# Kernel tuning notes

Hardware: AMD Instinct MI355X
Metric: run time of the kernel (lower is better)

The kernel has to match this reference:

```python
import jax, jax.numpy as jnp
import numpy as np

B, TK, NK, H = 64, 512, 256, 512

def _masked_renorm_softmax(scores, mask):
    # softmax over last dim, multiply by mask, renormalize (as in the torch code)
    p = jax.nn.softmax(scores, axis=-1) * mask
    return p / jnp.sum(p, axis=-1, keepdims=True)

def setup_inputs() -> dict:
    key = jax.random.key(0)
    ks = jax.random.split(key, 14)
    s = 0.02
    return {
        "s_t_hat": jax.random.normal(ks[0], (B, 2 * H), jnp.float32),
        "encoder_outputs_token": jax.random.normal(ks[1], (B, TK, H), jnp.float32),
        "encoder_outputs_node": jax.random.normal(ks[2], (B, NK, H), jnp.float32),
        "node_to_token": jax.random.randint(ks[3], (B, TK), 0, NK),
        "enc_padding_mask_token": jnp.ones((B, TK), jnp.float32),
        "enc_padding_mask_node": jnp.ones((B, NK), jnp.float32),
        "graph": jax.random.uniform(ks[4], (B, NK, NK), jnp.float32),
        "flow": jax.random.uniform(ks[5], (B, NK), jnp.float32),
        # parameters (Linear weights stored as [in, out]; x @ W == torch Linear)
        "W_c": jax.random.normal(ks[6], (H,), jnp.float32) * s,          # Linear(1, H)
        "W_tok": jax.random.normal(ks[7], (H, H), jnp.float32) * s,      # encode_proj_token
        "W_node": jax.random.normal(ks[8], (H, H), jnp.float32) * s,     # encode_proj_node
        "W_dec": jax.random.normal(ks[9], (2 * H, H), jnp.float32) * s,  # decode_proj
        "b_dec": jnp.zeros((H,), jnp.float32),
        "v_tok": jax.random.normal(ks[10], (H,), jnp.float32) * s,       # v_token
        "v_node": jax.random.normal(ks[11], (H,), jnp.float32) * s,      # v_node
    }

def reference(s_t_hat, encoder_outputs_token, encoder_outputs_node, node_to_token,
              enc_padding_mask_token, enc_padding_mask_node, graph, flow,
              W_c, W_tok, W_node, W_dec, b_dec, v_tok, v_node):
    # projections
    enc_tok_feat = jnp.einsum('bth,hk->btk', encoder_outputs_token, W_tok)   # [B,TK,H]
    enc_node_feat = jnp.einsum('bnh,hk->bnk', encoder_outputs_node, W_node)  # [B,NK,H]
    dec_fea = s_t_hat @ W_dec + b_dec                                        # [B,H]
    flow_feat = flow[..., None] * W_c                                        # [B,NK,H]

    # node attention
    e_node = jnp.tanh(enc_node_feat + dec_fea[:, None, :] + flow_feat)
    scores_node = jnp.einsum('bnh,h->bn', e_node, v_node)                    # [B,NK]
    attn_dist_node = _masked_renorm_softmax(scores_node, enc_padding_mask_node)

    # gather node attention onto tokens via node_to_token indices
    gathered = jnp.take_along_axis(attn_dist_node, node_to_token, axis=1)    # [B,TK]
    attn_dist_node_to_token = _masked_renorm_softmax(gathered, enc_padding_mask_token)

    # token attention
    e_tok = jnp.tanh(enc_tok_feat + dec_fea[:, None, :])
    scores_tok = jnp.einsum('bth,h->bt', e_tok, v_tok)                       # [B,TK]
    attn_dist_token = _masked_renorm_softmax(scores_tok, enc_padding_mask_token)

    # mix and context
    final_attn = 0.5 * attn_dist_token + 0.5 * attn_dist_node_to_token      # [B,TK]
    c_t = jnp.einsum('bt,bth->bh', final_attn, encoder_outputs_token)        # [B,H]

    # multi-hop graph diffusion of node attention
    zero_hop = attn_dist_node                                                # [B,NK]
    one_hop = jnp.einsum('bn,bnm->bm', zero_hop, graph)
    two_hop = jnp.einsum('bn,bnm->bm', one_hop, graph)
    flow_out = (zero_hop + one_hop + two_hop) * 0.33333

    return (c_t, final_attn, attn_dist_node, flow_out)
```

## Files before the change

kernel.cpp:

```cpp
#include <hip/hip_runtime.h>
#include <math.h>

constexpr int kB = 64;
constexpr int kTK = 512;
constexpr int kNK = 256;
constexpr int kH = 512;
constexpr int kTokBlocks = kB * kTK / 64;
constexpr int kNodeBlocks = kB * kNK / 64;

typedef float f32x4 __attribute__((ext_vector_type(4)));
typedef __bf16 bf16x8 __attribute__((ext_vector_type(8)));

__device__ __forceinline__ unsigned short f32_to_bf16(float f) {
  return (unsigned short)((__float_as_uint(f) + 0x8000u) >> 16);
}

__device__ __forceinline__ float tanh_fast(float x) {
  float e = __builtin_amdgcn_exp2f(x * 2.8853900817779268f);
  return 1.0f - 2.0f * __builtin_amdgcn_rcpf(e + 1.0f);
}

__device__ __forceinline__ void lds_barrier() {
  __builtin_amdgcn_s_waitcnt(0xC07F);
  __builtin_amdgcn_s_barrier();
}

__global__ __launch_bounds__(256) void prep_kernel(
    const float* __restrict__ Wtok, const float* __restrict__ Wnode,
    unsigned short* __restrict__ WtokT, unsigned short* __restrict__ WnodeT,
    const float* __restrict__ s_t_hat, const float* __restrict__ W_dec,
    float* __restrict__ dec_part) {
  __shared__ float sm[32 * 33];
  const int tid = threadIdx.x;
  if (blockIdx.x < 512) {
    const int idx = blockIdx.x;
    const int z = idx >> 8, rem = idx & 255;
    const int bx = rem & 15, by = rem >> 4;
    const float* W = z ? Wnode : Wtok;
    unsigned short* T = z ? WnodeT : WtokT;
    const int tx = tid & 31, ty = tid >> 5;
#pragma unroll
    for (int i = 0; i < 4; ++i)
      sm[(ty + 8 * i) * 33 + tx] =
          W[(size_t)(by * 32 + ty + 8 * i) * kH + bx * 32 + tx];
    __syncthreads();
#pragma unroll
    for (int i = 0; i < 4; ++i)
      T[(size_t)(bx * 32 + ty + 8 * i) * kH + by * 32 + tx] =
          f32_to_bf16(sm[tx * 33 + ty + 8 * i]);
  } else {
    const int r = blockIdx.x - 512;
    const int b = r >> 3, s = r & 7;
    if (tid < 128) sm[tid] = s_t_hat[(size_t)b * 1024 + s * 128 + tid];
    __syncthreads();
    float a0 = 0.f, a1 = 0.f;
    const float* w = W_dec + (size_t)(s * 128) * kH;
#pragma unroll 8
    for (int k = 0; k < 128; ++k) {
      a0 = fmaf(sm[k], w[(size_t)k * kH + tid], a0);
      a1 = fmaf(sm[k], w[(size_t)k * kH + tid + 256], a1);
    }
    dec_part[(size_t)(b * 8 + s) * kH + tid] = a0;
    dec_part[(size_t)(b * 8 + s) * kH + tid + 256] = a1;
  }
}

__global__ __launch_bounds__(1024, 4) void scores_fused_kernel(
    const float* __restrict__ enc_tok, const float* __restrict__ enc_node,
    const unsigned short* __restrict__ WtokT,
    const unsigned short* __restrict__ WnodeT,
    const float* __restrict__ dec_part, const float* __restrict__ b_dec,
    const float* __restrict__ flow, const float* __restrict__ W_c,
    const float* __restrict__ v_tok, const float* __restrict__ v_node,
    float* __restrict__ scores_tok, float* __restrict__ scores_node) {
  const int tid = threadIdx.x;
  const int wave = tid >> 6, lane = tid & 63;
  const int quad = lane >> 4, l15 = lane & 15;
  const bool is_node = blockIdx.x >= kTokBlocks;
  const int bidx = is_node ? (int)blockIdx.x - kTokBlocks : (int)blockIdx.x;
  const float* A = is_node ? enc_node : enc_tok;
  const unsigned short* WT = is_node ? WnodeT : WtokT;
  const float* v = is_node ? v_node : v_tok;
  float* scores = is_node ? scores_node : scores_tok;
  const int ROWS = is_node ? kNK : kTK;
  const int b = is_node ? (bidx >> 2) : (bidx >> 3);
  const int row0 = (is_node ? (bidx & 3) : (bidx & 7)) * 64;

  __shared__ __align__(16) unsigned short As[2][8192];
  __shared__ float red[16][64];

  const f32x4 fzero = {0.f, 0.f, 0.f, 0.f};
  f32x4 acc[4][2];
#pragma unroll
  for (int i = 0; i < 4; ++i)
#pragma unroll
    for (int j = 0; j < 2; ++j) acc[i][j] = fzero;

  const int r = tid >> 4;
  const int kcol = tid & 15;
  const float* aptr = A + (size_t)(b * ROWS + row0 + r) * kH + kcol * 4;
  const int k0 = kcol * 4;
  const int k1 = 64 + kcol * 4;
  const int s0 = ((k0 >> 5) * 4 + (r >> 4)) * 64 + ((k0 >> 3) & 3) * 16 + (r & 15);
  const int s1 = ((k1 >> 5) * 4 + (r >> 4)) * 64 + ((k1 >> 3) & 3) * 16 + (r & 15);
  const int sw0 = s0 ^ (((s0 >> 4) & 3) << 1) ^ ((s0 >> 8) & 1);
  const int sw1 = s1 ^ (((s1 >> 4) & 3) << 1) ^ ((s1 >> 8) & 1);
  const int addr0 = sw0 * 8 + (k0 & 7);
  const int addr1 = sw1 * 8 + (k1 & 7);

  float4 axA0, axA1, axB0, axB1;
  auto aloadA = [&](int kc) {
    axA0 = *(const float4*)(aptr + kc * 128);
    axA1 = *(const float4*)(aptr + kc * 128 + 64);
  };
  auto aloadB = [&](int kc) {
    axB0 = *(const float4*)(aptr + kc * 128);
    axB1 = *(const float4*)(aptr + kc * 128 + 64);
  };
  auto commit = [&](int buf, float4 x0, float4 x1) {
    ushort4 h0, h1;
    h0.x = f32_to_bf16(x0.x); h0.y = f32_to_bf16(x0.y);
    h0.z = f32_to_bf16(x0.z); h0.w = f32_to_bf16(x0.w);
    h1.x = f32_to_bf16(x1.x); h1.y = f32_to_bf16(x1.y);
    h1.z = f32_to_bf16(x1.z); h1.w = f32_to_bf16(x1.w);
    *(ushort4*)&As[buf][addr0] = h0;
    *(ushort4*)&As[buf][addr1] = h1;
  };

  const int n0 = wave * 32;
  const unsigned short* bbase = WT + (size_t)(n0 + l15) * kH + quad * 8;
  bf16x8 bbuf[4][2];
  auto loadB = [&](int sb, int g) {
    bbuf[sb][0] = *(const bf16x8*)(bbase + g * 32);
    bbuf[sb][1] = *(const bf16x8*)(bbase + (size_t)16 * kH + g * 32);
  };

  aloadA(0);
  aloadB(1);
  loadB(0, 0);
  loadB(1, 1);
  loadB(2, 2);
  commit(0, axA0, axA1);
  aloadA(2);
  lds_barrier();

#pragma unroll
  for (int g = 0; g < 16; ++g) {
    const int kc = g >> 2, kh = g & 3;
    if (g == 0) { commit(1, axB0, axB1); aloadB(3); }
    else if (g == 4) { commit(0, axA0, axA1); }
    else if (g == 8) { commit(1, axB0, axB1); }
    if (g < 13) loadB((g + 3) & 3, g + 3);
    bf16x8 afr[4];
#pragma unroll
    for (int mi = 0; mi < 4; ++mi) {
      const int slot = ((kh * 4 + mi) * 64 + lane) ^ (((lane >> 4) & 3) << 1) ^ (kh & 1);
      afr[mi] = *(const bf16x8*)&As[kc & 1][slot * 8];
    }
#pragma unroll
    for (int mi = 0; mi < 4; ++mi)
#pragma unroll
      for (int ni = 0; ni < 2; ++ni)
        acc[mi][ni] = __builtin_amdgcn_mfma_f32_16x16x32_bf16(
            afr[mi], bbuf[g & 3][ni], acc[mi][ni], 0, 0, 0);
    if (kh == 3 && kc < 3) lds_barrier();
  }

  float dec2[2], vv2[2], wc2[2];
#pragma unroll
  for (int ni = 0; ni < 2; ++ni) {
    const int col = n0 + 16 * ni + l15;
    float d = b_dec[col];
#pragma unroll
    for (int p = 0; p < 8; ++p) d += dec_part[(size_t)(b * 8 + p) * kH + col];
    dec2[ni] = d;
    vv2[ni] = v[col];
    wc2[ni] = is_node ? W_c[col] : 0.f;
  }
#pragma unroll
  for (int mi = 0; mi < 4; ++mi) {
#pragma unroll
    for (int reg = 0; reg < 4; ++reg) {
      const int row = 16 * mi + quad * 4 + reg;
      const float fl = is_node ? flow[b * kNK + row0 + row] : 0.f;
      float p = 0.f;
#pragma unroll
      for (int ni = 0; ni < 2; ++ni)
        p += tanh_fast(fmaf(fl, wc2[ni], acc[mi][ni][reg] + dec2[ni])) * vv2[ni];
#pragma unroll
      for (int off = 1; off < 16; off <<= 1) p += __shfl_xor(p, off, 64);
      if (l15 == 0) red[wave][row] = p;
    }
  }
  __syncthreads();
  if (tid < 64) {
    float s = 0.f;
#pragma unroll
    for (int w = 0; w < 16; ++w) s += red[w][tid];
    scores[b * ROWS + row0 + tid] = s;
  }
}

__device__ __forceinline__ float block_sum_512(float v, float* rbuf) {
#pragma unroll
  for (int off = 32; off >= 1; off >>= 1) v += __shfl_xor(v, off, 64);
  if ((threadIdx.x & 63) == 0) rbuf[threadIdx.x >> 6] = v;
  __syncthreads();
  float s = rbuf[0];
#pragma unroll
  for (int w = 1; w < 8; ++w) s += rbuf[w];
  __syncthreads();
  return s;
}

__global__ __launch_bounds__(512) void softmax_mix_kernel(
    const float* __restrict__ scores_node, const float* __restrict__ scores_tok,
    const int* __restrict__ node_to_token,
    const float* __restrict__ mask_tok, const float* __restrict__ mask_node,
    float* __restrict__ out_final, float* __restrict__ out_attn_node,
    float* __restrict__ out_flow) {
  const int b = blockIdx.x, tid = threadIdx.x;
  __shared__ float an_sh[kNK];
  __shared__ float rbuf[8];

  if (tid < kNK) out_flow[b * kNK + tid] = 0.f;

  float en = 0.f;
  if (tid < kNK)
    en = expf(scores_node[b * kNK + tid]) * mask_node[b * kNK + tid];
  float sn = block_sum_512(en, rbuf);
  float an = en / sn;
  if (tid < kNK) {
    an_sh[tid] = an;
    out_attn_node[b * kNK + tid] = an;
  }
  __syncthreads();

  const float mt = mask_tok[b * kTK + tid];
  const int idx = node_to_token[b * kTK + tid];
  float eg = expf(an_sh[idx]) * mt;
  float sg = block_sum_512(eg, rbuf);
  float an2t = eg / sg;

  float et = expf(scores_tok[b * kTK + tid]) * mt;
  float st = block_sum_512(et, rbuf);
  float at = et / st;

  out_final[b * kTK + tid] = 0.5f * (at + an2t);
}

__global__ __launch_bounds__(512) void ct_flow1_kernel(
    const float* __restrict__ final_attn, const float* __restrict__ enc_tok,
    const float* __restrict__ attn_node, const float* __restrict__ graph,
    float* __restrict__ ctp, float* __restrict__ fp1) {
  const int tid = threadIdx.x;
  if (blockIdx.x < 512) {
    const int b = blockIdx.x >> 3, s = blockIdx.x & 7;
    __shared__ float fa[64];
    __shared__ float part[4][512];
    if (tid < 64) fa[tid] = final_attn[b * kTK + s * 64 + tid];
    __syncthreads();
    const int h4 = (tid & 127) * 4, tsub = tid >> 7;
    float4 acc = {0.f, 0.f, 0.f, 0.f};
    const float* base =
        enc_tok + ((size_t)(b * kTK + s * 64 + tsub * 16)) * kH + h4;
#pragma unroll
    for (int t = 0; t < 16; ++t) {
      float4 e = *(const float4*)(base + (size_t)t * kH);
      const float w = fa[tsub * 16 + t];
      acc.x = fmaf(w, e.x, acc.x); acc.y = fmaf(w, e.y, acc.y);
      acc.z = fmaf(w, e.z, acc.z); acc.w = fmaf(w, e.w, acc.w);
    }
    *(float4*)&part[tsub][h4] = acc;
    __syncthreads();
    if (tid < 128) {
      float4 s0 = {0.f, 0.f, 0.f, 0.f};
#pragma unroll
      for (int p = 0; p < 4; ++p) {
        float4 pp = *(const float4*)&part[p][tid * 4];
        s0.x += pp.x; s0.y += pp.y; s0.z += pp.z; s0.w += pp.w;
      }
      *(float4*)&ctp[((size_t)(b * 8 + s)) * kH + tid * 4] = s0;
    }
  } else {
    const int rr = blockIdx.x - 512;
    const int b = rr >> 2, sl = rr & 3;
    __shared__ float z[64];
    __shared__ float part[8][256];
    if (tid < 64) z[tid] = attn_node[b * kNK + sl * 64 + tid];
    __syncthreads();
    const int m4 = (tid & 63) * 4, nsub = tid >> 6;
    float4 acc = {0.f, 0.f, 0.f, 0.f};
    const float* g =
        graph + ((size_t)(b * kNK + sl * 64 + nsub * 8)) * kNK + m4;
#pragma unroll
    for (int n = 0; n < 8; ++n) {
      float4 gg = *(const float4*)(g + (size_t)n * kNK);
      const float w = z[nsub * 8 + n];
      acc.x = fmaf(w, gg.x, acc.x); acc.y = fmaf(w, gg.y, acc.y);
      acc.z = fmaf(w, gg.z, acc.z); acc.w = fmaf(w, gg.w, acc.w);
    }
    *(float4*)&part[nsub][m4] = acc;
    __syncthreads();
    if (tid < 64) {
      float4 s0 = {0.f, 0.f, 0.f, 0.f};
#pragma unroll
      for (int p = 0; p < 8; ++p) {
        float4 pp = *(const float4*)&part[p][tid * 4];
        s0.x += pp.x; s0.y += pp.y; s0.z += pp.z; s0.w += pp.w;
      }
      *(float4*)&fp1[((size_t)(b * 4 + sl)) * kNK + tid * 4] = s0;
    }
  }
}

__global__ __launch_bounds__(512) void ct_flow2_kernel(
    const float* __restrict__ ctp, const float* __restrict__ fp1,
    const float* __restrict__ attn_node, const float* __restrict__ graph,
    float* __restrict__ out_ct, float* __restrict__ out_flow) {
  const int tid = threadIdx.x;
  if (blockIdx.x < 64) {
    const int b = blockIdx.x;
    __shared__ float acc_sh[4][512];
    const int h4 = (tid & 127) * 4, part = tid >> 7;
    float4 a = {0.f, 0.f, 0.f, 0.f};
#pragma unroll
    for (int j = 0; j < 2; ++j) {
      float4 c = *(const float4*)&ctp[((size_t)(b * 8 + part * 2 + j)) * kH + h4];
      a.x += c.x; a.y += c.y; a.z += c.z; a.w += c.w;
    }
    *(float4*)&acc_sh[part][h4] = a;
    __syncthreads();
    if (tid < 128) {
      float4 s = {0.f, 0.f, 0.f, 0.f};
#pragma unroll
      for (int p = 0; p < 4; ++p) {
        float4 pp = *(const float4*)&acc_sh[p][tid * 4];
        s.x += pp.x; s.y += pp.y; s.z += pp.z; s.w += pp.w;
      }
      *(float4*)&out_ct[b * kH + tid * 4] = s;
    }
  } else {
    const int rr = blockIdx.x - 64;
    const int b = rr >> 2, sl = rr & 3;
    __shared__ float one_sh[64];
    __shared__ float part2[8][256];
    if (tid < 64) {
      const int n = sl * 64 + tid;
      float one = 0.f;
#pragma unroll
      for (int p = 0; p < 4; ++p) one += fp1[((size_t)(b * 4 + p)) * kNK + n];
      one_sh[tid] = one;
      atomicAdd(&out_flow[b * kNK + n],
                (attn_node[b * kNK + n] + one) * 0.33333f);
    }
    __syncthreads();
    const int m4 = (tid & 63) * 4, nsub = tid >> 6;
    float4 acc = {0.f, 0.f, 0.f, 0.f};
    const float* g =
        graph + ((size_t)(b * kNK + sl * 64 + nsub * 8)) * kNK + m4;
#pragma unroll
    for (int n = 0; n < 8; ++n) {
      float4 gg = *(const float4*)(g + (size_t)n * kNK);
      const float w = one_sh[sl * 0 + nsub * 8 + n];
      acc.x = fmaf(w, gg.x, acc.x); acc.y = fmaf(w, gg.y, acc.y);
      acc.z = fmaf(w, gg.z, acc.z); acc.w = fmaf(w, gg.w, acc.w);
    }
    *(float4*)&part2[nsub][m4] = acc;
    __syncthreads();
    if (tid < 64) {
      float4 s = {0.f, 0.f, 0.f, 0.f};
#pragma unroll
      for (int p = 0; p < 8; ++p) {
        float4 pp = *(const float4*)&part2[p][tid * 4];
        s.x += pp.x; s.y += pp.y; s.z += pp.z; s.w += pp.w;
      }
      float* dst = &out_flow[b * kNK + tid * 4];
      atomicAdd(dst + 0, s.x * 0.33333f);
      atomicAdd(dst + 1, s.y * 0.33333f);
      atomicAdd(dst + 2, s.z * 0.33333f);
      atomicAdd(dst + 3, s.w * 0.33333f);
    }
  }
}

extern "C" void kernel_launch(void* const* d_in, const int* in_sizes, int n_in,
                              void* d_out, int out_size, void* d_ws, size_t ws_size,
                              hipStream_t stream) {
  (void)in_sizes; (void)n_in; (void)out_size; (void)ws_size;
  const float* s_t_hat  = (const float*)d_in[0];
  const float* enc_tok  = (const float*)d_in[1];
  const float* enc_node = (const float*)d_in[2];
  const int*   n2t      = (const int*)d_in[3];
  const float* mask_tok = (const float*)d_in[4];
  const float* mask_nd  = (const float*)d_in[5];
  const float* graph    = (const float*)d_in[6];
  const float* flow     = (const float*)d_in[7];
  const float* W_c      = (const float*)d_in[8];
  const float* W_tok    = (const float*)d_in[9];
  const float* W_node   = (const float*)d_in[10];
  const float* W_dec    = (const float*)d_in[11];
  const float* b_dec    = (const float*)d_in[12];
  const float* v_tok    = (const float*)d_in[13];
  const float* v_node   = (const float*)d_in[14];

  float* out = (float*)d_out;
  float* out_ct        = out;
  float* out_final     = out + kB * kH;
  float* out_attn_node = out + 2 * kB * kH;
  float* out_flow      = out_attn_node + kB * kNK;

  float* ws = (float*)d_ws;
  float* scores_tok  = ws;
  float* scores_node = ws + 32768;
  float* dec_part    = ws + 49152;
  float* ctp         = dec_part;
  float* fp1         = ws + 311296;
  unsigned short* WtokT  = (unsigned short*)(ws + 376832);
  unsigned short* WnodeT = WtokT + kH * kH;

  prep_kernel<<<1024, 256, 0, stream>>>(W_tok, W_node, WtokT, WnodeT,
                                        s_t_hat, W_dec, dec_part);
  scores_fused_kernel<<<kTokBlocks + kNodeBlocks, 1024, 0, stream>>>(
      enc_tok, enc_node, WtokT, WnodeT, dec_part, b_dec, flow, W_c,
      v_tok, v_node, scores_tok, scores_node);
  softmax_mix_kernel<<<kB, 512, 0, stream>>>(scores_node, scores_tok, n2t,
                                             mask_tok, mask_nd, out_final,
                                             out_attn_node, out_flow);
  ct_flow1_kernel<<<768, 512, 0, stream>>>(out_final, enc_tok, out_attn_node,
                                           graph, ctp, fp1);
  ct_flow2_kernel<<<320, 512, 0, stream>>>(ctp, fp1, out_attn_node, graph,
                                           out_ct, out_flow);
}
```

Before: 241.9 us.

## Halve waves per block in scores GEMM, widen per-wave N tile to 64

The fused scores kernel now runs 512 threads (8 waves) per block instead of 1024. Each wave computes a 64-column tile (4x4 MFMA accumulators), which doubles B-fragment reuse per A fragment. Each thread loads and converts two A rows per stage, and B prefetch depth drops from 4 stages to 2. The MFMA section is wrapped in s_setprio so matrix work gets issue priority. The cost is higher register pressure and less latency hiding from the shallower B prefetch.

```diff
diff --git a/kernel.cpp b/kernel.cpp
--- a/kernel.cpp
+++ b/kernel.cpp
@@ -65,7 +65,7 @@
   }
 }
 
-__global__ __launch_bounds__(1024, 4) void scores_fused_kernel(
+__global__ __launch_bounds__(512, 8) void scores_fused_kernel(
     const float* __restrict__ enc_tok, const float* __restrict__ enc_node,
     const unsigned short* __restrict__ WtokT,
     const unsigned short* __restrict__ WnodeT,
@@ -87,88 +87,94 @@
   const int row0 = (is_node ? (bidx & 3) : (bidx & 7)) * 64;
 
   __shared__ __align__(16) unsigned short As[2][8192];
-  __shared__ float red[16][64];
+  __shared__ float red[8][64];
 
   const f32x4 fzero = {0.f, 0.f, 0.f, 0.f};
-  f32x4 acc[4][2];
+  f32x4 acc[4][4];
 #pragma unroll
   for (int i = 0; i < 4; ++i)
 #pragma unroll
-    for (int j = 0; j < 2; ++j) acc[i][j] = fzero;
+    for (int j = 0; j < 4; ++j) acc[i][j] = fzero;
 
   const int r = tid >> 4;
   const int kcol = tid & 15;
   const float* aptr = A + (size_t)(b * ROWS + row0 + r) * kH + kcol * 4;
+  auto mkaddr = [](int row, int k) {
+    const int s = ((k >> 5) * 4 + (row >> 4)) * 64 + ((k >> 3) & 3) * 16 + (row & 15);
+    const int sw = s ^ (((s >> 4) & 3) << 1) ^ ((s >> 8) & 1);
+    return sw * 8 + (k & 7);
+  };
   const int k0 = kcol * 4;
   const int k1 = 64 + kcol * 4;
-  const int s0 = ((k0 >> 5) * 4 + (r >> 4)) * 64 + ((k0 >> 3) & 3) * 16 + (r & 15);
-  const int s1 = ((k1 >> 5) * 4 + (r >> 4)) * 64 + ((k1 >> 3) & 3) * 16 + (r & 15);
-  const int sw0 = s0 ^ (((s0 >> 4) & 3) << 1) ^ ((s0 >> 8) & 1);
-  const int sw1 = s1 ^ (((s1 >> 4) & 3) << 1) ^ ((s1 >> 8) & 1);
-  const int addr0 = sw0 * 8 + (k0 & 7);
-  const int addr1 = sw1 * 8 + (k1 & 7);
-
-  float4 axA0, axA1, axB0, axB1;
-  auto aloadA = [&](int kc) {
-    axA0 = *(const float4*)(aptr + kc * 128);
-    axA1 = *(const float4*)(aptr + kc * 128 + 64);
+  const int addr00 = mkaddr(r, k0), addr01 = mkaddr(r, k1);
+  const int addr10 = mkaddr(r + 32, k0), addr11 = mkaddr(r + 32, k1);
+
+  float4 ax0, ax1, ax2, ax3;
+  auto aload = [&](int kc) {
+    ax0 = *(const float4*)(aptr + kc * 128);
+    ax1 = *(const float4*)(aptr + kc * 128 + 64);
+    ax2 = *(const float4*)(aptr + (size_t)32 * kH + kc * 128);
+    ax3 = *(const float4*)(aptr + (size_t)32 * kH + kc * 128 + 64);
   };
-  auto aloadB = [&](int kc) {
-    axB0 = *(const float4*)(aptr + kc * 128);
-    axB1 = *(const float4*)(aptr + kc * 128 + 64);
+  auto commit = [&](int buf) {
+    ushort4 h0, h1, h2, h3;
+    h0.x = f32_to_bf16(ax0.x); h0.y = f32_to_bf16(ax0.y);
+    h0.z = f32_to_bf16(ax0.z); h0.w = f32_to_bf16(ax0.w);
+    h1.x = f32_to_bf16(ax1.x); h1.y = f32_to_bf16(ax1.y);
+    h1.z = f32_to_bf16(ax1.z); h1.w = f32_to_bf16(ax1.w);
+    h2.x = f32_to_bf16(ax2.x); h2.y = f32_to_bf16(ax2.y);
+    h2.z = f32_to_bf16(ax2.z); h2.w = f32_to_bf16(ax2.w);
+    h3.x = f32_to_bf16(ax3.x); h3.y = f32_to_bf16(ax3.y);
+    h3.z = f32_to_bf16(ax3.z); h3.w = f32_to_bf16(ax3.w);
+    *(ushort4*)&As[buf][addr00] = h0;
+    *(ushort4*)&As[buf][addr01] = h1;
+    *(ushort4*)&As[buf][addr10] = h2;
+    *(ushort4*)&As[buf][addr11] = h3;
   };
-  auto commit = [&](int buf, float4 x0, float4 x1) {
-    ushort4 h0, h1;
-    h0.x = f32_to_bf16(x0.x); h0.y = f32_to_bf16(x0.y);
-    h0.z = f32_to_bf16(x0.z); h0.w = f32_to_bf16(x0.w);
-    h1.x = f32_to_bf16(x1.x); h1.y = f32_to_bf16(x1.y);
-    h1.z = f32_to_bf16(x1.z); h1.w = f32_to_bf16(x1.w);
-    *(ushort4*)&As[buf][addr0] = h0;
-    *(ushort4*)&As[buf][addr1] = h1;
+
+  const int n0 = wave * 64;
+  const unsigned short* bbase = WT + (size_t)(n0 + l15) * kH + quad * 8;
+  bf16x8 bbuf[2][4];
+  auto loadB = [&](int sb, int g) {
+#pragma unroll
+    for (int ni = 0; ni < 4; ++ni)
+      bbuf[sb][ni] = *(const bf16x8*)(bbase + (size_t)(16 * ni) * kH + g * 32);
   };
 
-  const int n0 = wave * 32;
-  const unsigned short* bbase = WT + (size_t)(n0 + l15) * kH + quad * 8;
-  bf16x8 bbuf[4][2];
-  auto loadB = [&](int sb, int g) {
-    bbuf[sb][0] = *(const bf16x8*)(bbase + g * 32);
-    bbuf[sb][1] = *(const bf16x8*)(bbase + (size_t)16 * kH + g * 32);
-  };
-
-  aloadA(0);
-  aloadB(1);
+  aload(0);
+  commit(0);
+  aload(1);
   loadB(0, 0);
-  loadB(1, 1);
-  loadB(2, 2);
-  commit(0, axA0, axA1);
-  aloadA(2);
   lds_barrier();
 
 #pragma unroll
   for (int g = 0; g < 16; ++g) {
     const int kc = g >> 2, kh = g & 3;
-    if (g == 0) { commit(1, axB0, axB1); aloadB(3); }
-    else if (g == 4) { commit(0, axA0, axA1); }
-    else if (g == 8) { commit(1, axB0, axB1); }
-    if (g < 13) loadB((g + 3) & 3, g + 3);
+    if (kh == 0 && kc < 3) {
+      commit((kc + 1) & 1);
+      if (kc < 2) aload(kc + 2);
+    }
+    if (g < 15) loadB((g + 1) & 1, g + 1);
     bf16x8 afr[4];
 #pragma unroll
     for (int mi = 0; mi < 4; ++mi) {
       const int slot = ((kh * 4 + mi) * 64 + lane) ^ (((lane >> 4) & 3) << 1) ^ (kh & 1);
       afr[mi] = *(const bf16x8*)&As[kc & 1][slot * 8];
     }
+    __builtin_amdgcn_s_setprio(1);
 #pragma unroll
     for (int mi = 0; mi < 4; ++mi)
 #pragma unroll
-      for (int ni = 0; ni < 2; ++ni)
+      for (int ni = 0; ni < 4; ++ni)
         acc[mi][ni] = __builtin_amdgcn_mfma_f32_16x16x32_bf16(
-            afr[mi], bbuf[g & 3][ni], acc[mi][ni], 0, 0, 0);
+            afr[mi], bbuf[g & 1][ni], acc[mi][ni], 0, 0, 0);
+    __builtin_amdgcn_s_setprio(0);
     if (kh == 3 && kc < 3) lds_barrier();
   }
 
-  float dec2[2], vv2[2], wc2[2];
-#pragma unroll
-  for (int ni = 0; ni < 2; ++ni) {
+  float dec2[4], vv2[4], wc2[4];
+#pragma unroll
+  for (int ni = 0; ni < 4; ++ni) {
     const int col = n0 + 16 * ni + l15;
     float d = b_dec[col];
 #pragma unroll
@@ -185,7 +191,7 @@
       const float fl = is_node ? flow[b * kNK + row0 + row] : 0.f;
       float p = 0.f;
 #pragma unroll
-      for (int ni = 0; ni < 2; ++ni)
+      for (int ni = 0; ni < 4; ++ni)
         p += tanh_fast(fmaf(fl, wc2[ni], acc[mi][ni][reg] + dec2[ni])) * vv2[ni];
 #pragma unroll
       for (int off = 1; off < 16; off <<= 1) p += __shfl_xor(p, off, 64);
@@ -196,7 +202,7 @@
   if (tid < 64) {
     float s = 0.f;
 #pragma unroll
-    for (int w = 0; w < 16; ++w) s += red[w][tid];
+    for (int w = 0; w < 8; ++w) s += red[w][tid];
     scores[b * ROWS + row0 + tid] = s;
   }
 }
@@ -421,7 +427,7 @@
 
   prep_kernel<<<1024, 256, 0, stream>>>(W_tok, W_node, WtokT, WnodeT,
                                         s_t_hat, W_dec, dec_part);
-  scores_fused_kernel<<<kTokBlocks + kNodeBlocks, 1024, 0, stream>>>(
+  scores_fused_kernel<<<kTokBlocks + kNodeBlocks, 512, 0, stream>>>(
       enc_tok, enc_node, WtokT, WnodeT, dec_part, b_dec, flow, W_c,
       v_tok, v_node, scores_tok, scores_node);
   softmax_mix_kernel<<<kB, 512, 0, stream>>>(scores_node, scores_tok, n2t,
```

Result: slower. 843.0 us (+248.5%).
